# Optimization experiments

Hardware: AMD Instinct MI355X
Metric: run time of the kernel (lower is better)

Reference implementation:

```python
import jax, jax.numpy as jnp
import numpy as np

N_PTS0 = 32   # samples per line
N_PTS1 = 8    # after maxpool (scale factor 4)
DIM_LOI = 128
DIM_FC = 1024
FEAT_DIM = 8
HW = 128      # feature-map spatial size (hardcoded via clamp(max=127) in source)


def setup_inputs() -> dict:
    key = jax.random.key(0)
    ks = jax.random.split(key, 11)
    B, L = 8, 5000
    feature = jax.random.normal(ks[0], (B, 256, HW, HW), jnp.float32)
    # line endpoints in pixel coords [0, 128)
    p = jax.random.uniform(ks[1], (B, L, 2, 2), jnp.float32) * HW
    feat = jax.random.normal(ks[2], (B, L, FEAT_DIM), jnp.float32)
    W_fc1 = jax.random.normal(ks[3], (DIM_LOI, 256), jnp.float32) * 0.05
    b_fc1 = jnp.zeros((DIM_LOI,), jnp.float32)
    d_in = DIM_LOI * N_PTS1 + FEAT_DIM  # 1032
    W1 = jax.random.normal(ks[4], (d_in, DIM_FC), jnp.float32) * 0.03
    b1 = jnp.zeros((DIM_FC,), jnp.float32)
    W2 = jax.random.normal(ks[5], (DIM_FC, DIM_FC), jnp.float32) * 0.03
    b2 = jnp.zeros((DIM_FC,), jnp.float32)
    W3 = jax.random.normal(ks[6], (DIM_FC, 1), jnp.float32) * 0.03
    b3 = jnp.zeros((1,), jnp.float32)
    return dict(feature=feature, p=p, feat=feat, W_fc1=W_fc1, b_fc1=b_fc1,
                W1=W1, b1=b1, W2=W2, b2=b2, W3=W3, b3=b3)


def _loi_head(feature, p, feat, W_fc1, b_fc1, W1, b1, W2, b2, W3, b3):
    B, _, H, W = feature.shape
    L = p.shape[1]
    # fc1: 1x1 conv -> [B, DIM_LOI, H, W]
    x = jnp.einsum('bchw,dc->bdhw', feature, W_fc1) + b_fc1[None, :, None, None]

    # sample N_PTS0 points along each line: [B, L, 32, 2]
    lam = jnp.linspace(0.0, 1.0, N_PTS0, dtype=p.dtype)[:, None]
    pts = p[:, :, 0:1, :] * lam + p[:, :, 1:2, :] * (1.0 - lam) - 0.5
    px, py = pts[..., 0], pts[..., 1]
    px0 = jnp.clip(jnp.floor(px), 0.0, HW - 1)
    py0 = jnp.clip(jnp.floor(py), 0.0, HW - 1)
    px1 = jnp.clip(px0 + 1.0, 0.0, HW - 1)
    py1 = jnp.clip(py0 + 1.0, 0.0, HW - 1)
    px0i, py0i = px0.astype(jnp.int32), py0.astype(jnp.int32)
    px1i, py1i = px1.astype(jnp.int32), py1.astype(jnp.int32)

    # bilinear blend weights [B, L, 32] -> broadcast over channel dim
    w00 = ((px1 - px) * (py1 - py))[:, None]
    w10 = ((px - px0) * (py1 - py))[:, None]
    w01 = ((px1 - px) * (py - py0))[:, None]
    w11 = ((px - px0) * (py - py0))[:, None]

    gather = jax.vmap(lambda xb, ix, iy: xb[:, ix, iy])  # [C,L,32] per image
    xp = (gather(x, px0i, py0i) * w00 + gather(x, px1i, py0i) * w10 +
          gather(x, px0i, py1i) * w01 + gather(x, px1i, py1i) * w11)  # [B,C,L,32]
    xp = jnp.transpose(xp, (0, 2, 1, 3))  # [B, L, C, 32]

    # MaxPool1d(kernel=4, stride=4) over sampled points -> [B, L, C, 8]
    pooled = xp.reshape(B, L, DIM_LOI, N_PTS1, N_PTS0 // N_PTS1).max(-1)
    flat = pooled.reshape(B, L, DIM_LOI * N_PTS1)
    z = jnp.concatenate([flat, feat], axis=-1)  # [B, L, 1032]

    h = jax.nn.relu(z @ W1 + b1)
    h = jax.nn.relu(h @ W2 + b2)
    logits = (h @ W3 + b3)[..., 0]  # [B, L]
    return logits


def reference(feature, p, feat, W_fc1, b_fc1, W1, b1, W2, b2, W3, b3):
    return _loi_head(feature, p, feat, W_fc1, b_fc1, W1, b1, W2, b2, W3, b3)
```

## Files before the change

### kernel.cpp

```cpp
#include <hip/hip_runtime.h>

typedef _Float16 f16;
typedef __fp16 h16x2 __attribute__((ext_vector_type(2)));
typedef f16 f16x8 __attribute__((ext_vector_type(8)));
typedef float f32x4 __attribute__((ext_vector_type(4)));

#define HW    128
#define NPIX  16384
#define CDIM  256
#define DLOI  128
#define LROWS 40000
#define DFC   1024
#define KP1   1088

__global__ __launch_bounds__(256, 4) void conv1x1_kernel(
    const float* __restrict__ feature, const float* __restrict__ Wfc,
    const float* __restrict__ bfc, f16* __restrict__ x) {
  const int tid = threadIdx.x;
  const int l = tid & 63;
  const int w = tid >> 6;
  const int b = blockIdx.y;
  const int pix0 = blockIdx.x * 128;
  const int wr = (w >> 1) * 64;
  const int wc = (w & 1) * 64;
  const int lrow = l & 15;
  const int g4 = l >> 4;

  const float* fb = feature + (size_t)b * CDIM * NPIX;
  f32x4 acc[4][4] = {};

  for (int kf = 0; kf < 8; ++kf) {
    const int kb = kf * 32 + g4 * 8;
    f16x8 bf[4];
#pragma unroll
    for (int n = 0; n < 4; ++n) {
      const float* wp = &Wfc[(size_t)(wc + n * 16 + lrow) * CDIM + kb];
      float4 w0 = *(const float4*)wp;
      float4 w1 = *(const float4*)(wp + 4);
      union { f16x8 v; h16x2 h[4]; } u;
      u.h[0] = __builtin_amdgcn_cvt_pkrtz(w0.x, w0.y);
      u.h[1] = __builtin_amdgcn_cvt_pkrtz(w0.z, w0.w);
      u.h[2] = __builtin_amdgcn_cvt_pkrtz(w1.x, w1.y);
      u.h[3] = __builtin_amdgcn_cvt_pkrtz(w1.z, w1.w);
      bf[n] = u.v;
    }
#pragma unroll
    for (int m = 0; m < 4; ++m) {
      const int pix = pix0 + wr + m * 16 + lrow;
      const float* ap = fb + (size_t)kb * NPIX + pix;
      float av[8];
#pragma unroll
      for (int j = 0; j < 8; ++j) av[j] = ap[(size_t)j * NPIX];
      union { f16x8 v; h16x2 h[4]; } u;
      u.h[0] = __builtin_amdgcn_cvt_pkrtz(av[0], av[1]);
      u.h[1] = __builtin_amdgcn_cvt_pkrtz(av[2], av[3]);
      u.h[2] = __builtin_amdgcn_cvt_pkrtz(av[4], av[5]);
      u.h[3] = __builtin_amdgcn_cvt_pkrtz(av[6], av[7]);
#pragma unroll
      for (int n = 0; n < 4; ++n)
        acc[m][n] = __builtin_amdgcn_mfma_f32_16x16x32_f16(u.v, bf[n], acc[m][n], 0, 0, 0);
    }
  }

#pragma unroll
  for (int m = 0; m < 4; ++m) {
#pragma unroll
    for (int r = 0; r < 4; ++r) {
      const int pix = pix0 + wr + m * 16 + g4 * 4 + r;
      f16* xr = x + ((size_t)b * NPIX + pix) * DLOI;
#pragma unroll
      for (int n = 0; n < 4; ++n) {
        const int d = wc + n * 16 + lrow;
        xr[d] = (f16)(acc[m][n][r] + bfc[d]);
      }
    }
  }
}

__global__ __launch_bounds__(256) void sample_kernel(
    const f16* __restrict__ x, const float* __restrict__ p,
    const float* __restrict__ feat, f16* __restrict__ z) {
  const int tid = threadIdx.x;
  const int wv = tid >> 6;
  const int lane = tid & 63;
  const int sub = lane >> 4;
  const int cl = lane & 15;
  const int bid = blockIdx.x;
  const int b = bid & 7;
  const int row = b * 5000 + (bid >> 3) * 4 + wv;

  const float4 pe = *(const float4*)&p[(size_t)row * 4];
  const size_t bb = (size_t)b * NPIX;
  f16* zr = z + (size_t)row * KP1;

#pragma unroll
  for (int gh = 0; gh < 2; ++gh) {
    const int g = gh * 4 + sub;
    float acc[8];
#pragma unroll
    for (int ci = 0; ci < 8; ++ci) acc[ci] = -1e30f;
#pragma unroll
    for (int pt = 0; pt < 4; ++pt) {
      const int t = g * 4 + pt;
      const float lam = (float)t * (1.0f / 31.0f);
      const float px = pe.x * lam + pe.z * (1.f - lam) - 0.5f;
      const float py = pe.y * lam + pe.w * (1.f - lam) - 0.5f;
      const float px0 = fminf(fmaxf(floorf(px), 0.f), 127.f);
      const float py0 = fminf(fmaxf(floorf(py), 0.f), 127.f);
      const float px1 = fminf(px0 + 1.f, 127.f);
      const float py1 = fminf(py0 + 1.f, 127.f);
      const int ix0 = (int)px0, iy0 = (int)py0, ix1 = (int)px1, iy1 = (int)py1;
      const float w00 = (px1 - px) * (py1 - py);
      const float w10 = (px - px0) * (py1 - py);
      const float w01 = (px1 - px) * (py - py0);
      const float w11 = (px - px0) * (py - py0);

      const f16* r00 = x + (bb + ix0 * HW + iy0) * DLOI + cl * 8;
      const f16* r10 = x + (bb + ix1 * HW + iy0) * DLOI + cl * 8;
      const f16* r01 = x + (bb + ix0 * HW + iy1) * DLOI + cl * 8;
      const f16* r11 = x + (bb + ix1 * HW + iy1) * DLOI + cl * 8;
      f16x8 a  = *(const f16x8*)r00;
      f16x8 bq = *(const f16x8*)r10;
      f16x8 cq = *(const f16x8*)r01;
      f16x8 dq = *(const f16x8*)r11;
#pragma unroll
      for (int ci = 0; ci < 8; ++ci) {
        float m = w00 * (float)a[ci] + w10 * (float)bq[ci] +
                  w01 * (float)cq[ci] + w11 * (float)dq[ci];
        acc[ci] = fmaxf(acc[ci], m);
      }
    }
    f16x8 o;
#pragma unroll
    for (int ci = 0; ci < 8; ++ci) o[ci] = (f16)acc[ci];
    *(f16x8*)(zr + g * 128 + cl * 8) = o;
  }
  if (lane < 8) zr[1024 + lane] = (f16)feat[(size_t)row * 8 + lane];
  else if (lane < 36) *(unsigned int*)((char*)zr + 2064 + (lane - 8) * 4) = 0u;
}

__global__ __launch_bounds__(256) void wtrans_kernel(
    const float* __restrict__ W, f16* __restrict__ Wt, int K, int ldt, int permute) {
  __shared__ float t[32][33];
  const int tx = threadIdx.x & 31, ty = threadIdx.x >> 5;
#pragma unroll
  for (int i = 0; i < 4; ++i) {
    int kd = blockIdx.y * 32 + ty + i * 8;
    int ks = (permute && kd < 1024) ? ((kd & 127) * 8 + (kd >> 7)) : kd;
    int n = blockIdx.x * 32 + tx;
    t[ty + i * 8][tx] = (ks < K) ? W[(size_t)ks * DFC + n] : 0.f;
  }
  __syncthreads();
#pragma unroll
  for (int i = 0; i < 4; ++i) {
    int n = blockIdx.x * 32 + ty + i * 8;
    int k = blockIdx.y * 32 + tx;
    Wt[(size_t)n * ldt + k] = (f16)t[tx][ty + i * 8];
  }
}

#define GEMM_MAIN_LOOP(A_, Bt_, M_, ksteps_, lda_)                              \
  __shared__ f16 As[256 * 64];                                                  \
  __shared__ f16 Bs[128 * 64];                                                  \
  const int tid = threadIdx.x;                                                  \
  const int l = tid & 63;                                                       \
  const int w = tid >> 6;                                                       \
  const int nwg = gridDim.x;                                  \
  const int s = (blockIdx.x & 7) * (nwg >> 3) + (blockIdx.x >> 3);              \
  const int m0 = (s >> 3) * 256;                                                \
  const int n0 = (s & 7) * 128;                                                 \
  const int wr = (w >> 1) * 64, wc = (w & 1) * 64;                              \
  const int srow = tid >> 3;                                         \
  const int slot = tid & 7;                                                     \
  const int lrow = l & 15, g4 = l >> 4;                                         \
  f32x4 acc[4][4] = {};                                                         \
  for (int kt = 0; kt < ksteps_; ++kt) {                                        \
    const int kb = kt * 64;                                                     \
    __syncthreads();                                                            \
    _Pragma("unroll")                                                           \
    for (int c = 0; c < 4; ++c) {                                               \
      int row = c * 64 + srow;                                                  \
      int arow = m0 + row; if (arow >= M_) arow = M_ - 1;                       \
      const f16* g = A_ + (size_t)arow * lda_ + kb + ((slot ^ (row & 7)) * 8);  \
      __builtin_amdgcn_global_load_lds(                                         \
          (const __attribute__((address_space(1))) void*)g,                     \
          (__attribute__((address_space(3))) void*)(As + row * 64 + slot * 8),  \
          16, 0, 0);                                                            \
    }                                                                           \
    _Pragma("unroll")                                                           \
    for (int c = 0; c < 2; ++c) {                                               \
      int row = c * 64 + srow;                                                  \
      const f16* g = Bt_ + (size_t)(n0 + row) * lda_ + kb + ((slot ^ (row & 7)) * 8); \
      __builtin_amdgcn_global_load_lds(                                         \
          (const __attribute__((address_space(1))) void*)g,                     \
          (__attribute__((address_space(3))) void*)(Bs + row * 64 + slot * 8),  \
          16, 0, 0);                                                            \
    }                                                                           \
    __syncthreads();                                                            \
    _Pragma("unroll")                                                           \
    for (int kh = 0; kh < 2; ++kh) {                                            \
      f16x8 af[4], bf[4];                                                       \
      _Pragma("unroll")                                                         \
      for (int m = 0; m < 4; ++m) {                                             \
        int row = wr + m * 16 + lrow;                                           \
        int sl = (g4 + 4 * kh) ^ (row & 7);                                     \
        af[m] = *(const f16x8*)(As + row * 64 + sl * 8);                        \
      }                                                                         \
      _Pragma("unroll")                                                         \
      for (int n = 0; n < 4; ++n) {                                             \
        int row = wc + n * 16 + lrow;                                           \
        int sl = (g4 + 4 * kh) ^ (row & 7);                                     \
        bf[n] = *(const f16x8*)(Bs + row * 64 + sl * 8);                        \
      }                                                                         \
      _Pragma("unroll")                                                         \
      for (int m = 0; m < 4; ++m)                                               \
        _Pragma("unroll")                                                       \
        for (int n = 0; n < 4; ++n)                                             \
          acc[m][n] = __builtin_amdgcn_mfma_f32_16x16x32_f16(af[m], bf[n], acc[m][n], 0, 0, 0); \
    }                                                                           \
  }

__global__ __launch_bounds__(512, 4) void gemm_f16(
    const f16* __restrict__ A, const f16* __restrict__ Bt,
    const float* __restrict__ bias, f16* __restrict__ C,
    int M, int ksteps, int lda) {
  GEMM_MAIN_LOOP(A, Bt, M, ksteps, lda)

  const int ocol0 = n0 + wc + lrow;
  const int orow0 = m0 + wr + g4 * 4;
#pragma unroll
  for (int m = 0; m < 4; ++m) {
#pragma unroll
    for (int r = 0; r < 4; ++r) {
      int orow = orow0 + m * 16 + r;
      if (orow >= M) continue;
      f16* crow = C + (size_t)orow * DFC;
#pragma unroll
      for (int n = 0; n < 4; ++n) {
        int col = ocol0 + n * 16;
        float v = acc[m][n][r] + bias[col];
        crow[col] = (f16)fmaxf(v, 0.f);
      }
    }
  }
}

__global__ __launch_bounds__(512, 4) void gemm2_fc3(
    const f16* __restrict__ A, const f16* __restrict__ Bt,
    const float* __restrict__ bias, const float* __restrict__ W3,
    float* __restrict__ out, int M, int ksteps, int lda) {
  GEMM_MAIN_LOOP(A, Bt, M, ksteps, lda)

  const int ocol0 = n0 + wc + lrow;
  const int orow0 = m0 + wr + g4 * 4;
  float b4[4], w3v[4];
#pragma unroll
  for (int n = 0; n < 4; ++n) {
    b4[n] = bias[ocol0 + n * 16];
    w3v[n] = W3[ocol0 + n * 16];
  }
#pragma unroll
  for (int m = 0; m < 4; ++m) {
#pragma unroll
    for (int r = 0; r < 4; ++r) {
      float sacc = 0.f;
#pragma unroll
      for (int n = 0; n < 4; ++n) {
        float v = fmaxf(acc[m][n][r] + b4[n], 0.f);
        sacc += v * w3v[n];
      }
      sacc += __shfl_xor(sacc, 1);
      sacc += __shfl_xor(sacc, 2);
      sacc += __shfl_xor(sacc, 4);
      sacc += __shfl_xor(sacc, 8);
      int orow = orow0 + m * 16 + r;
      if (lrow == 0 && orow < M) atomicAdd(&out[orow], sacc);
    }
  }
}

__global__ __launch_bounds__(256) void fill_out(
    float* __restrict__ out, const float* __restrict__ b3, int n) {
  int i = blockIdx.x * 256 + threadIdx.x;
  if (i < n) out[i] = b3[0];
}

extern "C" void kernel_launch(void* const* d_in, const int* in_sizes, int n_in,
                              void* d_out, int out_size, void* d_ws, size_t ws_size,
                              hipStream_t stream) {
  const float* feature = (const float*)d_in[0];
  const float* p       = (const float*)d_in[1];
  const float* feat    = (const float*)d_in[2];
  const float* W_fc1   = (const float*)d_in[3];
  const float* b_fc1   = (const float*)d_in[4];
  const float* W1      = (const float*)d_in[5];
  const float* b1      = (const float*)d_in[6];
  const float* W2      = (const float*)d_in[7];
  const float* b2      = (const float*)d_in[8];
  const float* W3      = (const float*)d_in[9];
  const float* b3      = (const float*)d_in[10];
  float* out = (float*)d_out;

  char* ws = (char*)d_ws;
  f16* x   = (f16*)(ws + 0);
  f16* z   = (f16*)(ws + 33554432ULL);
  f16* h1  = (f16*)(ws + 120594432ULL);
  f16* W1t = (f16*)(ws + 202514432ULL);
  f16* W2t = (f16*)(ws + 204742656ULL);

  hipLaunchKernelGGL(wtrans_kernel, dim3(32, 34), dim3(256), 0, stream,
                     W1, W1t, 1032, KP1, 1);
  hipLaunchKernelGGL(wtrans_kernel, dim3(32, 32), dim3(256), 0, stream,
                     W2, W2t, 1024, 1024, 0);
  hipLaunchKernelGGL(conv1x1_kernel, dim3(128, 8), dim3(256), 0, stream,
                     feature, W_fc1, b_fc1, x);
  hipLaunchKernelGGL(sample_kernel, dim3(10000), dim3(256), 0, stream,
                     x, p, feat, z);
  hipLaunchKernelGGL(gemm_f16, dim3(1256), dim3(512), 0, stream,
                     z, W1t, b1, h1, LROWS, KP1 / 64, KP1);
  hipLaunchKernelGGL(fill_out, dim3(157), dim3(256), 0, stream,
                     out, b3, LROWS);
  hipLaunchKernelGGL(gemm2_fc3, dim3(1256), dim3(512), 0, stream,
                     h1, W2t, b2, W3, out, LROWS, DFC / 64, DFC);
}
```

Before: 339.1 us.

## Split 1x1 conv into fp16 transpose pass and LDS-staged MFMA GEMM

```diff
diff --git a/kernel.cpp b/kernel.cpp
--- a/kernel.cpp
+++ b/kernel.cpp
@@ -13,65 +13,120 @@
 #define DFC   1024
 #define KP1   1088
 
-__global__ __launch_bounds__(256, 4) void conv1x1_kernel(
-    const float* __restrict__ feature, const float* __restrict__ Wfc,
-    const float* __restrict__ bfc, f16* __restrict__ x) {
+__global__ __launch_bounds__(256) void wcast_kernel(
+    const float* __restrict__ W, f16* __restrict__ Wc, int n) {
+  int i = blockIdx.x * 256 + threadIdx.x;
+  if (i < n) Wc[i] = (f16)W[i];
+}
+
+__global__ __launch_bounds__(256) void transpose_kernel(
+    const float* __restrict__ feature, f16* __restrict__ ft) {
+  __shared__ float t[64][65];
+  const int tid = threadIdx.x;
+  const int bid = blockIdx.x;
+  const int b = bid & 7;
+  const int tile = bid >> 3;
+  const int pix0 = (tile & 255) * 64;
+  const int c0 = (tile >> 8) * 64;
+
+  const float* fb = feature + ((size_t)b * CDIM + c0) * NPIX + pix0;
+#pragma unroll
+  for (int i = 0; i < 4; ++i) {
+    const int c = (tid >> 4) + i * 16;
+    const int px = (tid & 15) * 4;
+    float4 v = *(const float4*)(fb + (size_t)c * NPIX + px);
+    t[c][px] = v.x; t[c][px + 1] = v.y; t[c][px + 2] = v.z; t[c][px + 3] = v.w;
+  }
+  __syncthreads();
+  f16* fo = ft + ((size_t)b * NPIX + pix0) * CDIM + c0;
+#pragma unroll
+  for (int i = 0; i < 2; ++i) {
+    const int px = (tid >> 3) + i * 32;
+    const int co = (tid & 7) * 8;
+    float v[8];
+#pragma unroll
+    for (int j = 0; j < 8; ++j) v[j] = t[co + j][px];
+    union { f16x8 o; h16x2 h[4]; } u;
+    u.h[0] = __builtin_amdgcn_cvt_pkrtz(v[0], v[1]);
+    u.h[1] = __builtin_amdgcn_cvt_pkrtz(v[2], v[3]);
+    u.h[2] = __builtin_amdgcn_cvt_pkrtz(v[4], v[5]);
+    u.h[3] = __builtin_amdgcn_cvt_pkrtz(v[6], v[7]);
+    *(f16x8*)(fo + (size_t)px * CDIM + co) = u.o;
+  }
+}
+
+__global__ __launch_bounds__(512, 4) void conv_gemm(
+    const f16* __restrict__ A, const f16* __restrict__ Bt,
+    const float* __restrict__ bias, f16* __restrict__ C) {
+  __shared__ f16 As[256 * 64];
+  __shared__ f16 Bs[128 * 64];
   const int tid = threadIdx.x;
   const int l = tid & 63;
   const int w = tid >> 6;
-  const int b = blockIdx.y;
-  const int pix0 = blockIdx.x * 128;
-  const int wr = (w >> 1) * 64;
-  const int wc = (w & 1) * 64;
-  const int lrow = l & 15;
-  const int g4 = l >> 4;
-
-  const float* fb = feature + (size_t)b * CDIM * NPIX;
+  const int s = (blockIdx.x & 7) * 64 + (blockIdx.x >> 3);
+  const int m0 = s * 256;
+  const int wr = (w >> 1) * 64, wc = (w & 1) * 64;
+  const int srow = tid >> 3;
+  const int slot = tid & 7;
+  const int lrow = l & 15, g4 = l >> 4;
   f32x4 acc[4][4] = {};
 
-  for (int kf = 0; kf < 8; ++kf) {
-    const int kb = kf * 32 + g4 * 8;
-    f16x8 bf[4];
-#pragma unroll
-    for (int n = 0; n < 4; ++n) {
-      const float* wp = &Wfc[(size_t)(wc + n * 16 + lrow) * CDIM + kb];
-      float4 w0 = *(const float4*)wp;
-      float4 w1 = *(const float4*)(wp + 4);
-      union { f16x8 v; h16x2 h[4]; } u;
-      u.h[0] = __builtin_amdgcn_cvt_pkrtz(w0.x, w0.y);
-      u.h[1] = __builtin_amdgcn_cvt_pkrtz(w0.z, w0.w);
-      u.h[2] = __builtin_amdgcn_cvt_pkrtz(w1.x, w1.y);
-      u.h[3] = __builtin_amdgcn_cvt_pkrtz(w1.z, w1.w);
-      bf[n] = u.v;
-    }
-#pragma unroll
-    for (int m = 0; m < 4; ++m) {
-      const int pix = pix0 + wr + m * 16 + lrow;
-      const float* ap = fb + (size_t)kb * NPIX + pix;
-      float av[8];
-#pragma unroll
-      for (int j = 0; j < 8; ++j) av[j] = ap[(size_t)j * NPIX];
-      union { f16x8 v; h16x2 h[4]; } u;
-      u.h[0] = __builtin_amdgcn_cvt_pkrtz(av[0], av[1]);
-      u.h[1] = __builtin_amdgcn_cvt_pkrtz(av[2], av[3]);
-      u.h[2] = __builtin_amdgcn_cvt_pkrtz(av[4], av[5]);
-      u.h[3] = __builtin_amdgcn_cvt_pkrtz(av[6], av[7]);
-#pragma unroll
-      for (int n = 0; n < 4; ++n)
-        acc[m][n] = __builtin_amdgcn_mfma_f32_16x16x32_f16(u.v, bf[n], acc[m][n], 0, 0, 0);
-    }
-  }
-
+  for (int kt = 0; kt < 4; ++kt) {
+    const int kb = kt * 64;
+    __syncthreads();
+#pragma unroll
+    for (int c = 0; c < 4; ++c) {
+      int row = c * 64 + srow;
+      const f16* g = A + (size_t)(m0 + row) * CDIM + kb + ((slot ^ (row & 7)) * 8);
+      __builtin_amdgcn_global_load_lds(
+          (const __attribute__((address_space(1))) void*)g,
+          (__attribute__((address_space(3))) void*)(As + row * 64 + slot * 8),
+          16, 0, 0);
+    }
+#pragma unroll
+    for (int c = 0; c < 2; ++c) {
+      int row = c * 64 + srow;
+      const f16* g = Bt + (size_t)row * CDIM + kb + ((slot ^ (row & 7)) * 8);
+      __builtin_amdgcn_global_load_lds(
+          (const __attribute__((address_space(1))) void*)g,
+          (__attribute__((address_space(3))) void*)(Bs + row * 64 + slot * 8),
+          16, 0, 0);
+    }
+    __syncthreads();
+#pragma unroll
+    for (int kh = 0; kh < 2; ++kh) {
+      f16x8 af[4], bf[4];
+#pragma unroll
+      for (int m = 0; m < 4; ++m) {
+        int row = wr + m * 16 + lrow;
+        int sl = (g4 + 4 * kh) ^ (row & 7);
+        af[m] = *(const f16x8*)(As + row * 64 + sl * 8);
+      }
+#pragma unroll
+      for (int n = 0; n < 4; ++n) {
+        int row = wc + n * 16 + lrow;
+        int sl = (g4 + 4 * kh) ^ (row & 7);
+        bf[n] = *(const f16x8*)(Bs + row * 64 + sl * 8);
+      }
+#pragma unroll
+      for (int m = 0; m < 4; ++m)
+#pragma unroll
+        for (int n = 0; n < 4; ++n)
+          acc[m][n] = __builtin_amdgcn_mfma_f32_16x16x32_f16(af[m], bf[n], acc[m][n], 0, 0, 0);
+    }
+  }
+
+  const int ocol0 = wc + lrow;
+  const int orow0 = m0 + wr + g4 * 4;
 #pragma unroll
   for (int m = 0; m < 4; ++m) {
 #pragma unroll
     for (int r = 0; r < 4; ++r) {
-      const int pix = pix0 + wr + m * 16 + g4 * 4 + r;
-      f16* xr = x + ((size_t)b * NPIX + pix) * DLOI;
+      f16* crow = C + (size_t)(orow0 + m * 16 + r) * DLOI;
 #pragma unroll
       for (int n = 0; n < 4; ++n) {
-        const int d = wc + n * 16 + lrow;
-        xr[d] = (f16)(acc[m][n][r] + bfc[d]);
+        int col = ocol0 + n * 16;
+        crow[col] = (f16)(acc[m][n][r] + bias[col]);
       }
     }
   }
@@ -302,18 +357,24 @@
   float* out = (float*)d_out;
 
   char* ws = (char*)d_ws;
-  f16* x   = (f16*)(ws + 0);
-  f16* z   = (f16*)(ws + 33554432ULL);
-  f16* h1  = (f16*)(ws + 120594432ULL);
-  f16* W1t = (f16*)(ws + 202514432ULL);
-  f16* W2t = (f16*)(ws + 204742656ULL);
-
+  f16* x    = (f16*)(ws + 0);
+  f16* z    = (f16*)(ws + 33554432ULL);
+  f16* h1   = (f16*)(ws + 120594432ULL);
+  f16* W1t  = (f16*)(ws + 202514432ULL);
+  f16* W2t  = (f16*)(ws + 204742656ULL);
+  f16* Wc16 = (f16*)(ws + 206839808ULL);
+  f16* ft   = h1;
+
+  hipLaunchKernelGGL(wcast_kernel, dim3(128), dim3(256), 0, stream,
+                     W_fc1, Wc16, DLOI * CDIM);
   hipLaunchKernelGGL(wtrans_kernel, dim3(32, 34), dim3(256), 0, stream,
                      W1, W1t, 1032, KP1, 1);
   hipLaunchKernelGGL(wtrans_kernel, dim3(32, 32), dim3(256), 0, stream,
                      W2, W2t, 1024, 1024, 0);
-  hipLaunchKernelGGL(conv1x1_kernel, dim3(128, 8), dim3(256), 0, stream,
-                     feature, W_fc1, b_fc1, x);
+  hipLaunchKernelGGL(transpose_kernel, dim3(8192), dim3(256), 0, stream,
+                     feature, ft);
+  hipLaunchKernelGGL(conv_gemm, dim3(512), dim3(512), 0, stream,
+                     ft, Wc16, b_fc1, x);
   hipLaunchKernelGGL(sample_kernel, dim3(10000), dim3(256), 0, stream,
                      x, p, feat, z);
   hipLaunchKernelGGL(gemm_f16, dim3(1256), dim3(512), 0, stream,
```

New measurement: 328.9 us. -3.0%, faster.

## Stage feature tile in LDS as fp16 with swizzle for conv1x1

Applied to the files above, without the earlier changes.

```diff
diff --git a/kernel.cpp b/kernel.cpp
--- a/kernel.cpp
+++ b/kernel.cpp
@@ -13,28 +13,49 @@
 #define DFC   1024
 #define KP1   1088
 
-__global__ __launch_bounds__(256, 4) void conv1x1_kernel(
+__global__ __launch_bounds__(256, 4) void fused_conv(
     const float* __restrict__ feature, const float* __restrict__ Wfc,
     const float* __restrict__ bfc, f16* __restrict__ x) {
+  __shared__ unsigned int t16[64 * 128];
   const int tid = threadIdx.x;
   const int l = tid & 63;
   const int w = tid >> 6;
-  const int b = blockIdx.y;
-  const int pix0 = blockIdx.x * 128;
-  const int wr = (w >> 1) * 64;
-  const int wc = (w & 1) * 64;
-  const int lrow = l & 15;
-  const int g4 = l >> 4;
+  const int bid = blockIdx.x;
+  const int b = bid & 7;
+  const int pix0 = (bid >> 3) * 64;
+  const int lrow = l & 15, g4 = l >> 4;
 
   const float* fb = feature + (size_t)b * CDIM * NPIX;
-  f32x4 acc[4][4] = {};
-
+
+  const int cpb = tid >> 4;
+  const int px4 = (tid & 15) * 4;
+#pragma unroll
+  for (int pass = 0; pass < 8; ++pass) {
+    const int cp = cpb + pass * 16;
+    const float* r0 = fb + (size_t)(2 * cp) * NPIX + pix0 + px4;
+    float4 a = *(const float4*)r0;
+    float4 c = *(const float4*)(r0 + NPIX);
+    union { h16x2 h; unsigned int u; } v[4];
+    v[0].h = __builtin_amdgcn_cvt_pkrtz(a.x, c.x);
+    v[1].h = __builtin_amdgcn_cvt_pkrtz(a.y, c.y);
+    v[2].h = __builtin_amdgcn_cvt_pkrtz(a.z, c.z);
+    v[3].h = __builtin_amdgcn_cvt_pkrtz(a.w, c.w);
+#pragma unroll
+    for (int i = 0; i < 4; ++i) {
+      const int pix = px4 + i;
+      t16[pix * 128 + (cp ^ (4 * (pix & 7)))] = v[i].u;
+    }
+  }
+  __syncthreads();
+
+  f32x4 acc[4][2] = {};
+#pragma unroll
   for (int kf = 0; kf < 8; ++kf) {
     const int kb = kf * 32 + g4 * 8;
-    f16x8 bf[4];
-#pragma unroll
-    for (int n = 0; n < 4; ++n) {
-      const float* wp = &Wfc[(size_t)(wc + n * 16 + lrow) * CDIM + kb];
+    f16x8 bf[2];
+#pragma unroll
+    for (int n = 0; n < 2; ++n) {
+      const float* wp = &Wfc[(size_t)(w * 32 + n * 16 + lrow) * CDIM + kb];
       float4 w0 = *(const float4*)wp;
       float4 w1 = *(const float4*)(wp + 4);
       union { f16x8 v; h16x2 h[4]; } u;
@@ -44,21 +65,14 @@
       u.h[3] = __builtin_amdgcn_cvt_pkrtz(w1.z, w1.w);
       bf[n] = u.v;
     }
+    const int cp0 = kf * 16 + g4 * 4;
 #pragma unroll
     for (int m = 0; m < 4; ++m) {
-      const int pix = pix0 + wr + m * 16 + lrow;
-      const float* ap = fb + (size_t)kb * NPIX + pix;
-      float av[8];
-#pragma unroll
-      for (int j = 0; j < 8; ++j) av[j] = ap[(size_t)j * NPIX];
-      union { f16x8 v; h16x2 h[4]; } u;
-      u.h[0] = __builtin_amdgcn_cvt_pkrtz(av[0], av[1]);
-      u.h[1] = __builtin_amdgcn_cvt_pkrtz(av[2], av[3]);
-      u.h[2] = __builtin_amdgcn_cvt_pkrtz(av[4], av[5]);
-      u.h[3] = __builtin_amdgcn_cvt_pkrtz(av[6], av[7]);
-#pragma unroll
-      for (int n = 0; n < 4; ++n)
-        acc[m][n] = __builtin_amdgcn_mfma_f32_16x16x32_f16(u.v, bf[n], acc[m][n], 0, 0, 0);
+      const int pix = m * 16 + lrow;
+      const f16x8 af = *(const f16x8*)(t16 + pix * 128 + (cp0 ^ (4 * (pix & 7))));
+#pragma unroll
+      for (int n = 0; n < 2; ++n)
+        acc[m][n] = __builtin_amdgcn_mfma_f32_16x16x32_f16(af, bf[n], acc[m][n], 0, 0, 0);
     }
   }
 
@@ -66,11 +80,11 @@
   for (int m = 0; m < 4; ++m) {
 #pragma unroll
     for (int r = 0; r < 4; ++r) {
-      const int pix = pix0 + wr + m * 16 + g4 * 4 + r;
+      const int pix = pix0 + m * 16 + g4 * 4 + r;
       f16* xr = x + ((size_t)b * NPIX + pix) * DLOI;
 #pragma unroll
-      for (int n = 0; n < 4; ++n) {
-        const int d = wc + n * 16 + lrow;
+      for (int n = 0; n < 2; ++n) {
+        const int d = w * 32 + n * 16 + lrow;
         xr[d] = (f16)(acc[m][n][r] + bfc[d]);
       }
     }
@@ -302,17 +316,17 @@
   float* out = (float*)d_out;
 
   char* ws = (char*)d_ws;
-  f16* x   = (f16*)(ws + 0);
-  f16* z   = (f16*)(ws + 33554432ULL);
-  f16* h1  = (f16*)(ws + 120594432ULL);
-  f16* W1t = (f16*)(ws + 202514432ULL);
-  f16* W2t = (f16*)(ws + 204742656ULL);
+  f16* x    = (f16*)(ws + 0);
+  f16* z    = (f16*)(ws + 33554432ULL);
+  f16* h1   = (f16*)(ws + 120594432ULL);
+  f16* W1t  = (f16*)(ws + 202514432ULL);
+  f16* W2t  = (f16*)(ws + 204742656ULL);
 
   hipLaunchKernelGGL(wtrans_kernel, dim3(32, 34), dim3(256), 0, stream,
                      W1, W1t, 1032, KP1, 1);
   hipLaunchKernelGGL(wtrans_kernel, dim3(32, 32), dim3(256), 0, stream,
                      W2, W2t, 1024, 1024, 0);
-  hipLaunchKernelGGL(conv1x1_kernel, dim3(128, 8), dim3(256), 0, stream,
+  hipLaunchKernelGGL(fused_conv, dim3(2048), dim3(256), 0, stream,
                      feature, W_fc1, b_fc1, x);
   hipLaunchKernelGGL(sample_kernel, dim3(10000), dim3(256), 0, stream,
                      x, p, feat, z);
```

Measured after the change: 320.6 us. 1.06x faster.
